# Performance work log

Measured on AMD Instinct MI355X. Metric: run time of the kernel, lower is better.

The kernel has to match this reference:

```python
import jax, jax.numpy as jnp
import numpy as np

DT = 0.01
B = 2097152
STATE_DIM, LATENT_DIM, INPUT_DIM = 3, 4, 3
TOTAL = STATE_DIM + LATENT_DIM  # 7
HID_L, HID_B = 64, 32


def setup_inputs() -> dict:
    key = jax.random.key(0)
    ks = jax.random.split(key, 16)
    def w(k, shape, fan_in):
        return (jax.random.normal(k, shape, dtype=jnp.float32) / np.sqrt(fan_in)).astype(jnp.float32)
    return {
        "state": jax.random.normal(ks[0], (B, TOTAL), dtype=jnp.float32),
        "u": jax.random.normal(ks[1], (B, INPUT_DIM), dtype=jnp.float32),
        # linear physics prior: s_dot = s@A.T + u@Bm.T ; y_phys = s@C.T
        "A": w(ks[2], (STATE_DIM, STATE_DIM), STATE_DIM),
        "Bm": w(ks[3], (STATE_DIM, INPUT_DIM), INPUT_DIM),
        "C": w(ks[4], (STATE_DIM, STATE_DIM), STATE_DIM),
        # z_gate: Linear(10 -> 7) + sigmoid
        "Wz": w(ks[5], (TOTAL, TOTAL + INPUT_DIM), TOTAL + INPUT_DIM),
        "bz": jnp.full((TOTAL,), 2.0, dtype=jnp.float32),
        # latent_dyn: Linear(10 -> 64) tanh Linear(64 -> 4)
        "W1": w(ks[6], (HID_L, TOTAL + INPUT_DIM), TOTAL + INPUT_DIM),
        "b1": jnp.zeros((HID_L,), dtype=jnp.float32),
        "W2": w(ks[7], (LATENT_DIM, HID_L), HID_L),
        "b2": jnp.zeros((LATENT_DIM,), dtype=jnp.float32),
        # 3 branches stacked: Linear(6 -> 32) tanh Linear(32 -> 1)
        "Wb1": w(ks[8], (3, HID_B, STATE_DIM + INPUT_DIM), STATE_DIM + INPUT_DIM),
        "bb1": jnp.zeros((3, HID_B), dtype=jnp.float32),
        "Wb2": w(ks[9], (3, HID_B), HID_B),
        "bb2": jnp.zeros((3,), dtype=jnp.float32),
    }


def reference(state, u, A, Bm, C, Wz, bz, W1, b1, W2, b2, Wb1, bb1, Wb2, bb2):
    s = state[:, :STATE_DIM]          # [B,3]
    latent = state[:, STATE_DIM:]     # [B,4]
    # physics prior
    s_dot_phys = s @ A.T + u @ Bm.T   # [B,3]
    y_phys = s @ C.T                  # [B,3]
    s_phys_next = s + DT * s_dot_phys
    su = jnp.concatenate([state, u], axis=1)  # [B,10]
    # latent dynamics
    latent_dot = jnp.tanh(su @ W1.T + b1) @ W2.T + b2   # [B,4]
    latent_next = latent + DT * latent_dot
    candidate = jnp.concatenate([s_phys_next, latent_next], axis=1)  # [B,7]
    # update gate
    z = jax.nn.sigmoid(su @ Wz.T + bz)                  # [B,7]
    next_state = z * candidate + (1.0 - z) * state
    # residual branch heads (vectorized over the 3 heads)
    branch_in = jnp.concatenate([s, u], axis=1)         # [B,6]
    h = jnp.tanh(jnp.einsum('bi,khi->bkh', branch_in, Wb1) + bb1)  # [B,3,32]
    residuals = jnp.einsum('bkh,kh->bk', h, Wb2) + bb2  # [B,3]
    y = y_phys + residuals
    return (next_state, y)
```

## Files before the change

### kernel.cpp

```cpp
#include <hip/hip_runtime.h>


#define DT_C 0.01f
#define NROWS 2097152
#define LOG2E 1.44269504088896340736f

__device__ __forceinline__ float fast_exp(float x) {
    return __builtin_amdgcn_exp2f(x * LOG2E);
}
__device__ __forceinline__ float fast_tanh(float x) {
    float e = __builtin_amdgcn_exp2f(x * (2.0f * LOG2E));
    return 1.0f - 2.0f * __builtin_amdgcn_rcpf(1.0f + e);
}
__device__ __forceinline__ float fast_sigmoid(float x) {
    float e = __builtin_amdgcn_exp2f(-x * LOG2E);
    return __builtin_amdgcn_rcpf(1.0f + e);
}

__global__ __launch_bounds__(256) void phygru_kernel(
    const float* __restrict__ state, const float* __restrict__ u,
    const float* __restrict__ A,     const float* __restrict__ Bm,
    const float* __restrict__ C,     const float* __restrict__ Wz,
    const float* __restrict__ bz,    const float* __restrict__ W1,
    const float* __restrict__ b1,    const float* __restrict__ W2,
    const float* __restrict__ b2,    const float* __restrict__ Wb1,
    const float* __restrict__ bb1,   const float* __restrict__ Wb2,
    const float* __restrict__ bb2,   float* __restrict__ out)
{
    const int row = blockIdx.x * blockDim.x + threadIdx.x;

    float st[7];
    #pragma unroll
    for (int i = 0; i < 7; ++i) st[i] = state[row * 7 + i];
    float uu[3];
    #pragma unroll
    for (int i = 0; i < 3; ++i) uu[i] = u[row * 3 + i];

    float su[10];
    #pragma unroll
    for (int i = 0; i < 7; ++i) su[i] = st[i];
    #pragma unroll
    for (int i = 0; i < 3; ++i) su[7 + i] = uu[i];

    float sp[3], yp[3];
    #pragma unroll
    for (int i = 0; i < 3; ++i) {
        float sd = 0.0f;
        #pragma unroll
        for (int j = 0; j < 3; ++j) sd = fmaf(A[i * 3 + j], st[j], sd);
        #pragma unroll
        for (int j = 0; j < 3; ++j) sd = fmaf(Bm[i * 3 + j], uu[j], sd);
        float y = 0.0f;
        #pragma unroll
        for (int j = 0; j < 3; ++j) y = fmaf(C[i * 3 + j], st[j], y);
        sp[i] = fmaf(DT_C, sd, st[i]);
        yp[i] = y;
    }

    float ld[4] = { b2[0], b2[1], b2[2], b2[3] };
    #pragma unroll
    for (int h = 0; h < 64; ++h) {
        float a = b1[h];
        #pragma unroll
        for (int i = 0; i < 10; ++i) a = fmaf(W1[h * 10 + i], su[i], a);
        float t = fast_tanh(a);
        #pragma unroll
        for (int k = 0; k < 4; ++k) ld[k] = fmaf(W2[k * 64 + h], t, ld[k]);
    }
    float ln[4];
    #pragma unroll
    for (int k = 0; k < 4; ++k) ln[k] = fmaf(DT_C, ld[k], st[3 + k]);

    float ns[7];
    #pragma unroll
    for (int j = 0; j < 7; ++j) {
        float a = bz[j];
        #pragma unroll
        for (int i = 0; i < 10; ++i) a = fmaf(Wz[j * 10 + i], su[i], a);
        float z = fast_sigmoid(a);
        float cand = (j < 3) ? sp[j] : ln[j - 3];
        ns[j] = fmaf(z, cand - st[j], st[j]);
    }

    float bi[6] = { st[0], st[1], st[2], uu[0], uu[1], uu[2] };
    float res[3];
    #pragma unroll
    for (int k = 0; k < 3; ++k) {
        float r = bb2[k];
        #pragma unroll
        for (int h = 0; h < 32; ++h) {
            float a = bb1[k * 32 + h];
            #pragma unroll
            for (int i = 0; i < 6; ++i)
                a = fmaf(Wb1[(k * 32 + h) * 6 + i], bi[i], a);
            r = fmaf(Wb2[k * 32 + h], fast_tanh(a), r);
        }
        res[k] = r;
    }

    #pragma unroll
    for (int j = 0; j < 7; ++j) out[row * 7 + j] = ns[j];
    float* yout = out + (size_t)NROWS * 7;
    #pragma unroll
    for (int k = 0; k < 3; ++k) yout[row * 3 + k] = yp[k] + res[k];
}

extern "C" void kernel_launch(void* const* d_in, const int* in_sizes, int n_in,
                              void* d_out, int out_size, void* d_ws, size_t ws_size,
                              hipStream_t stream) {
    const float* state = (const float*)d_in[0];
    const float* u     = (const float*)d_in[1];
    const float* A     = (const float*)d_in[2];
    const float* Bm    = (const float*)d_in[3];
    const float* C     = (const float*)d_in[4];
    const float* Wz    = (const float*)d_in[5];
    const float* bz    = (const float*)d_in[6];
    const float* W1    = (const float*)d_in[7];
    const float* b1    = (const float*)d_in[8];
    const float* W2    = (const float*)d_in[9];
    const float* b2    = (const float*)d_in[10];
    const float* Wb1   = (const float*)d_in[11];
    const float* bb1   = (const float*)d_in[12];
    const float* Wb2   = (const float*)d_in[13];
    const float* bb2   = (const float*)d_in[14];
    float* out = (float*)d_out;

    dim3 grid(NROWS / 256), block(256);
    phygru_kernel<<<grid, block, 0, stream>>>(
        state, u, A, Bm, C, Wz, bz, W1, b1, W2, b2, Wb1, bb1, Wb2, bb2, out);
}
```

Baseline: 307.8 us.

## Use packed fp16 dot2 for MLP layers with prescaled weights from prep kernel

Adds a small prep kernel that packs the weights into fp16 pairs and folds the exp2 scaling constants (2*log2e for tanh, -log2e for sigmoid) into the weights and biases, writing the result to workspace. The main kernel converts the inputs to packed fp16 and uses v_dot2 (fdot2) for every matvec, roughly halving the FMA instruction count in this compute-bound kernel. It also removes the per-activation multiply before exp2. The cost is fp16 rounding of inputs, weights and the hidden tanh values, which may loosen accuracy, plus one extra small kernel launch.

Measured after the change: 259.7 us. 1.19x faster.

```diff
diff --git a/kernel.cpp b/kernel.cpp
--- a/kernel.cpp
+++ b/kernel.cpp
@@ -1,34 +1,117 @@
 #include <hip/hip_runtime.h>
+#include <stdint.h>
 
 
 #define DT_C 0.01f
 #define NROWS 2097152
-#define LOG2E 1.44269504088896340736f
-
-__device__ __forceinline__ float fast_exp(float x) {
-    return __builtin_amdgcn_exp2f(x * LOG2E);
-}
-__device__ __forceinline__ float fast_tanh(float x) {
-    float e = __builtin_amdgcn_exp2f(x * (2.0f * LOG2E));
-    return 1.0f - 2.0f * __builtin_amdgcn_rcpf(1.0f + e);
-}
-__device__ __forceinline__ float fast_sigmoid(float x) {
-    float e = __builtin_amdgcn_exp2f(-x * LOG2E);
+#define LOG2E 1.4426950408889634f
+#define S2L   2.8853901617779268f
+
+typedef __fp16 h2 __attribute__((ext_vector_type(2)));
+
+__device__ __forceinline__ h2 pkrtz(float a, float b) {
+    return __builtin_amdgcn_cvt_pkrtz(a, b);
+}
+
+#if __has_builtin(__builtin_amdgcn_fdot2)
+__device__ __forceinline__ float fdot2(h2 a, h2 b, float c) {
+    return __builtin_amdgcn_fdot2(a, b, c, false);
+}
+#else
+__device__ __forceinline__ float fdot2(h2 a, h2 b, float c) {
+    return fmaf((float)a[0], (float)b[0], fmaf((float)a[1], (float)b[1], c));
+}
+#endif
+
+__device__ __forceinline__ float tanh_pre(float xs) {
+    float e = __builtin_amdgcn_exp2f(xs);
+    return fmaf(-2.0f, __builtin_amdgcn_rcpf(1.0f + e), 1.0f);
+}
+__device__ __forceinline__ float sigmoid_pre(float xs) {
+    float e = __builtin_amdgcn_exp2f(xs);
     return __builtin_amdgcn_rcpf(1.0f + e);
+}
+
+#define W1P_OFF   0
+#define WZP_OFF   320
+#define WB1P_OFF  355
+#define W2P_OFF   643
+#define PHYSP_OFF 771
+#define CP_OFF    780
+#define B1S_OFF   786
+#define BZS_OFF   850
+#define BB1S_OFF  857
+
+__device__ __forceinline__ uint32_t pack2(float a, float b) {
+    h2 v = pkrtz(a, b);
+    uint32_t u; __builtin_memcpy(&u, &v, 4); return u;
+}
+
+__global__ void prep_kernel(const float* __restrict__ A, const float* __restrict__ Bm,
+                            const float* __restrict__ C, const float* __restrict__ Wz,
+                            const float* __restrict__ bz, const float* __restrict__ W1,
+                            const float* __restrict__ b1, const float* __restrict__ Wb1,
+                            const float* __restrict__ bb1, const float* __restrict__ W2,
+                            uint32_t* __restrict__ ws)
+{
+    const int tid = blockIdx.x * blockDim.x + threadIdx.x;
+    const int nt = gridDim.x * blockDim.x;
+    float* wsf = (float*)ws;
+
+    for (int i = tid; i < 320; i += nt) {
+        int h = i / 5, j = i % 5;
+        ws[W1P_OFF + i] = pack2(W1[h*10 + 2*j] * S2L, W1[h*10 + 2*j + 1] * S2L);
+    }
+    for (int i = tid; i < 35; i += nt) {
+        int r = i / 5, j = i % 5;
+        ws[WZP_OFF + i] = pack2(Wz[r*10 + 2*j] * -LOG2E, Wz[r*10 + 2*j + 1] * -LOG2E);
+    }
+    for (int i = tid; i < 288; i += nt) {
+        int row = i / 3, j = i % 3;
+        ws[WB1P_OFF + i] = pack2(Wb1[row*6 + 2*j] * S2L, Wb1[row*6 + 2*j + 1] * S2L);
+    }
+    for (int i = tid; i < 128; i += nt) {
+        int k = i / 32, j = i % 32;
+        ws[W2P_OFF + i] = pack2(W2[k*64 + 2*j], W2[k*64 + 2*j + 1]);
+    }
+    for (int i = tid; i < 9; i += nt) {
+        int r = i / 3, j = i % 3;
+        float a, b;
+        if (j == 0) { a = A[r*3+0];  b = A[r*3+1];  }
+        else if (j == 1) { a = A[r*3+2];  b = Bm[r*3+0]; }
+        else { a = Bm[r*3+1]; b = Bm[r*3+2]; }
+        ws[PHYSP_OFF + i] = pack2(a, b);
+    }
+    for (int i = tid; i < 6; i += nt) {
+        int r = i / 2, j = i % 2;
+        float a = (j == 0) ? C[r*3+0] : C[r*3+2];
+        float b = (j == 0) ? C[r*3+1] : 0.0f;
+        ws[CP_OFF + i] = pack2(a, b);
+    }
+    for (int i = tid; i < 64; i += nt) wsf[B1S_OFF + i] = b1[i] * S2L;
+    for (int i = tid; i < 7;  i += nt) wsf[BZS_OFF + i] = bz[i] * -LOG2E;
+    for (int i = tid; i < 96; i += nt) wsf[BB1S_OFF + i] = bb1[i] * S2L;
 }
 
 __global__ __launch_bounds__(256) void phygru_kernel(
     const float* __restrict__ state, const float* __restrict__ u,
-    const float* __restrict__ A,     const float* __restrict__ Bm,
-    const float* __restrict__ C,     const float* __restrict__ Wz,
-    const float* __restrict__ bz,    const float* __restrict__ W1,
-    const float* __restrict__ b1,    const float* __restrict__ W2,
-    const float* __restrict__ b2,    const float* __restrict__ Wb1,
-    const float* __restrict__ bb1,   const float* __restrict__ Wb2,
-    const float* __restrict__ bb2,   float* __restrict__ out)
+    const uint32_t* __restrict__ ws, const float* __restrict__ b2,
+    const float* __restrict__ Wb2,   const float* __restrict__ bb2,
+    float* __restrict__ out)
 {
     const int row = blockIdx.x * blockDim.x + threadIdx.x;
 
+    const h2* W1p  = (const h2*)(ws + W1P_OFF);
+    const h2* Wzp  = (const h2*)(ws + WZP_OFF);
+    const h2* Wb1p = (const h2*)(ws + WB1P_OFF);
+    const h2* W2p  = (const h2*)(ws + W2P_OFF);
+    const h2* Pp   = (const h2*)(ws + PHYSP_OFF);
+    const h2* Cp   = (const h2*)(ws + CP_OFF);
+    const float* wsf  = (const float*)ws;
+    const float* b1s  = wsf + B1S_OFF;
+    const float* bzs  = wsf + BZS_OFF;
+    const float* bb1s = wsf + BB1S_OFF;
+
     float st[7];
     #pragma unroll
     for (int i = 0; i < 7; ++i) st[i] = state[row * 7 + i];
@@ -36,64 +119,71 @@
     #pragma unroll
     for (int i = 0; i < 3; ++i) uu[i] = u[row * 3 + i];
 
-    float su[10];
-    #pragma unroll
-    for (int i = 0; i < 7; ++i) su[i] = st[i];
-    #pragma unroll
-    for (int i = 0; i < 3; ++i) su[7 + i] = uu[i];
+    h2 suh[5];
+    suh[0] = pkrtz(st[0], st[1]);
+    suh[1] = pkrtz(st[2], st[3]);
+    suh[2] = pkrtz(st[4], st[5]);
+    suh[3] = pkrtz(st[6], uu[0]);
+    suh[4] = pkrtz(uu[1], uu[2]);
+    h2 bih[3];
+    bih[0] = suh[0];
+    bih[1] = pkrtz(st[2], uu[0]);
+    bih[2] = suh[4];
 
     float sp[3], yp[3];
     #pragma unroll
-    for (int i = 0; i < 3; ++i) {
-        float sd = 0.0f;
+    for (int r = 0; r < 3; ++r) {
+        float sd = fdot2(Pp[r*3+0], bih[0],
+                   fdot2(Pp[r*3+1], bih[1],
+                   fdot2(Pp[r*3+2], bih[2], 0.0f)));
+        sp[r] = fmaf(DT_C, sd, st[r]);
+        yp[r] = fdot2(Cp[r*2+0], bih[0], fdot2(Cp[r*2+1], bih[1], 0.0f));
+    }
+
+    float ld0 = b2[0], ld1 = b2[1], ld2 = b2[2], ld3 = b2[3];
+    #pragma unroll
+    for (int hp = 0; hp < 32; ++hp) {
+        const int h0 = 2 * hp, h1 = 2 * hp + 1;
+        float a0 = b1s[h0], a1 = b1s[h1];
         #pragma unroll
-        for (int j = 0; j < 3; ++j) sd = fmaf(A[i * 3 + j], st[j], sd);
+        for (int j = 0; j < 5; ++j) {
+            a0 = fdot2(W1p[h0*5 + j], suh[j], a0);
+            a1 = fdot2(W1p[h1*5 + j], suh[j], a1);
+        }
+        h2 th = pkrtz(tanh_pre(a0), tanh_pre(a1));
+        ld0 = fdot2(W2p[0*32 + hp], th, ld0);
+        ld1 = fdot2(W2p[1*32 + hp], th, ld1);
+        ld2 = fdot2(W2p[2*32 + hp], th, ld2);
+        ld3 = fdot2(W2p[3*32 + hp], th, ld3);
+    }
+    float ln[4];
+    ln[0] = fmaf(DT_C, ld0, st[3]);
+    ln[1] = fmaf(DT_C, ld1, st[4]);
+    ln[2] = fmaf(DT_C, ld2, st[5]);
+    ln[3] = fmaf(DT_C, ld3, st[6]);
+
+    float ns[7];
+    #pragma unroll
+    for (int j = 0; j < 7; ++j) {
+        float a = bzs[j];
         #pragma unroll
-        for (int j = 0; j < 3; ++j) sd = fmaf(Bm[i * 3 + j], uu[j], sd);
-        float y = 0.0f;
-        #pragma unroll
-        for (int j = 0; j < 3; ++j) y = fmaf(C[i * 3 + j], st[j], y);
-        sp[i] = fmaf(DT_C, sd, st[i]);
-        yp[i] = y;
-    }
-
-    float ld[4] = { b2[0], b2[1], b2[2], b2[3] };
-    #pragma unroll
-    for (int h = 0; h < 64; ++h) {
-        float a = b1[h];
-        #pragma unroll
-        for (int i = 0; i < 10; ++i) a = fmaf(W1[h * 10 + i], su[i], a);
-        float t = fast_tanh(a);
-        #pragma unroll
-        for (int k = 0; k < 4; ++k) ld[k] = fmaf(W2[k * 64 + h], t, ld[k]);
-    }
-    float ln[4];
-    #pragma unroll
-    for (int k = 0; k < 4; ++k) ln[k] = fmaf(DT_C, ld[k], st[3 + k]);
-
-    float ns[7];
-    #pragma unroll
-    for (int j = 0; j < 7; ++j) {
-        float a = bz[j];
-        #pragma unroll
-        for (int i = 0; i < 10; ++i) a = fmaf(Wz[j * 10 + i], su[i], a);
-        float z = fast_sigmoid(a);
+        for (int i = 0; i < 5; ++i) a = fdot2(Wzp[j*5 + i], suh[i], a);
+        float z = sigmoid_pre(a);
         float cand = (j < 3) ? sp[j] : ln[j - 3];
         ns[j] = fmaf(z, cand - st[j], st[j]);
     }
 
-    float bi[6] = { st[0], st[1], st[2], uu[0], uu[1], uu[2] };
     float res[3];
     #pragma unroll
     for (int k = 0; k < 3; ++k) {
         float r = bb2[k];
         #pragma unroll
         for (int h = 0; h < 32; ++h) {
-            float a = bb1[k * 32 + h];
+            float a = bb1s[k*32 + h];
             #pragma unroll
-            for (int i = 0; i < 6; ++i)
-                a = fmaf(Wb1[(k * 32 + h) * 6 + i], bi[i], a);
-            r = fmaf(Wb2[k * 32 + h], fast_tanh(a), r);
+            for (int j = 0; j < 3; ++j)
+                a = fdot2(Wb1p[(k*32 + h)*3 + j], bih[j], a);
+            r = fmaf(Wb2[k*32 + h], tanh_pre(a), r);
         }
         res[k] = r;
     }
@@ -124,8 +214,8 @@
     const float* Wb2   = (const float*)d_in[13];
     const float* bb2   = (const float*)d_in[14];
     float* out = (float*)d_out;
-
-    dim3 grid(NROWS / 256), block(256);
-    phygru_kernel<<<grid, block, 0, stream>>>(
-        state, u, A, Bm, C, Wz, bz, W1, b1, W2, b2, Wb1, bb1, Wb2, bb2, out);
-}
+    uint32_t* ws = (uint32_t*)d_ws;
+
+    prep_kernel<<<4, 256, 0, stream>>>(A, Bm, C, Wz, bz, W1, b1, Wb1, bb1, W2, ws);
+    phygru_kernel<<<NROWS / 256, 256, 0, stream>>>(state, u, ws, b2, Wb2, bb2, out);
+}
```
